# Kernel tuning notes

Measured on AMD Instinct MI355X. Metric: run time of the kernel, lower is better.

The kernel has to match this reference:

```python
import jax, jax.numpy as jnp
import numpy as np

B, T, C = 256, 2048, 39   # batch, time, nb_filters
NB = 8                     # number of dilation levels (2**0 .. 2**7)
K = 2                      # kernel size
NC = 8                     # num_classes
EPS = 1e-5                 # BatchNorm eps (eval mode)


def _causal_conv(x, w, b, d):
    """x: [B,C,T], w: [Cout,Cin,K], left-pad (K-1)*d for causality."""
    k = w.shape[-1]
    y = jax.lax.conv_general_dilated(
        x, w, window_strides=(1,), padding=[((k - 1) * d, 0)],
        rhs_dilation=(d,), dimension_numbers=('NCH', 'OIH', 'NCH'))
    return y + b[None, :, None]


def _bn(x, g, be, m, v):
    # eval-mode BatchNorm1d with running stats
    return g[None, :, None] * (x - m[None, :, None]) * jax.lax.rsqrt(v + EPS)[None, :, None] + be[None, :, None]


def _block(x, w, b, g, be, m, v, d):
    # Temporal_Aware_Block, eval mode (dropout = identity).
    # w: [2,C,C,K], b/g/be/m/v: [2,C]
    y = jax.nn.relu(_bn(_causal_conv(x, w[0], b[0], d), g[0], be[0], m[0], v[0]))
    y = jax.nn.relu(_bn(_causal_conv(y, w[1], b[1], d), g[1], be[1], m[1], v[1]))
    # causal conv preserves length, so the 1x1 residual conv branch is never taken
    return x * jax.nn.sigmoid(y)


def setup_inputs() -> dict:
    key = jax.random.key(0)
    ks = jax.random.split(key, 24)
    f = lambda k, s: jax.random.normal(k, s, dtype=jnp.float32) * 0.1
    return {
        'inputs': jax.random.normal(ks[0], (B, T, C), dtype=jnp.float32),
        'conv1x1_w': f(ks[1], (C, C, 1)),
        'conv1x1_b': f(ks[2], (C,)),
        'fw_conv_w': f(ks[3], (NB, 2, C, C, K)),
        'fw_conv_b': f(ks[4], (NB, 2, C)),
        'fw_gamma': 1.0 + f(ks[5], (NB, 2, C)),
        'fw_beta': f(ks[6], (NB, 2, C)),
        'fw_mean': f(ks[7], (NB, 2, C)),
        'fw_var': jax.random.uniform(ks[8], (NB, 2, C), dtype=jnp.float32, minval=0.5, maxval=1.5),
        'bw_conv_w': f(ks[9], (NB, 2, C, C, K)),
        'bw_conv_b': f(ks[10], (NB, 2, C)),
        'bw_gamma': 1.0 + f(ks[11], (NB, 2, C)),
        'bw_beta': f(ks[12], (NB, 2, C)),
        'bw_mean': f(ks[13], (NB, 2, C)),
        'bw_var': jax.random.uniform(ks[14], (NB, 2, C), dtype=jnp.float32, minval=0.5, maxval=1.5),
        'wl_kernel': f(ks[15], (NB, 1)),
        'cls_w': f(ks[16], (NC, C)),
        'cls_b': f(ks[17], (NC,)),
    }


def reference(inputs, conv1x1_w, conv1x1_b,
              fw_conv_w, fw_conv_b, fw_gamma, fw_beta, fw_mean, fw_var,
              bw_conv_w, bw_conv_b, bw_gamma, bw_beta, bw_mean, bw_var,
              wl_kernel, cls_w, cls_b):
    x = jnp.transpose(inputs, (0, 2, 1))           # [B,C,T]
    fwd = _causal_conv(x, conv1x1_w, conv1x1_b, 1)
    bwd = _causal_conv(x[:, :, ::-1], conv1x1_w, conv1x1_b, 1)
    skips = []
    for i in range(NB):
        d = 2 ** i
        fwd = _block(fwd, fw_conv_w[i], fw_conv_b[i], fw_gamma[i], fw_beta[i], fw_mean[i], fw_var[i], d)
        bwd = _block(bwd, bw_conv_w[i], bw_conv_b[i], bw_gamma[i], bw_beta[i], bw_mean[i], bw_var[i], d)
        skips.append(jnp.mean(fwd + bwd, axis=-1))  # [B,C]
    g = jnp.stack(skips, axis=-1)                   # [B,C,NB]
    x2 = jnp.einsum('bcn,no->bc', g, wl_kernel)     # WeightLayer matmul + squeeze
    logits = x2 @ cls_w.T + cls_b                   # [B,NC]
    return jax.nn.log_softmax(logits, axis=1)
```

## Files before the change

kernel.cpp:

```cpp
#include <hip/hip_runtime.h>
#include <math.h>

#define BATCH 256
#define TT    2048
#define CC    39
#define CP    40
#define NBLK  8
#define KK    2
#define NCLS  8
#define BN_EPS 1e-5f

typedef __attribute__((ext_vector_type(8))) short short8;
typedef __attribute__((ext_vector_type(4))) float floatx4;

__device__ __forceinline__ unsigned short f2b(float f) {
    union { float f; unsigned u; } v; v.f = f;
    unsigned r = v.u + 0x7FFF + ((v.u >> 16) & 1);
    return (unsigned short)(r >> 16);
}
__device__ __forceinline__ float b2f(unsigned short h) {
    union { unsigned u; float f; } v; v.u = ((unsigned)h) << 16;
    return v.f;
}

#define WFB_PER_BLKDIR (2*2*2*3*512)
#define WFB_TOTAL      (2*NBLK*WFB_PER_BLKDIR)
#define BFB_TOTAL      (2*NBLK*2*48)
#define WFF_TOTAL      (2*3*512)
#define BFF_TOTAL      48

__global__ void fold_kernel(const float* __restrict__ fw_w, const float* __restrict__ fw_b,
                            const float* __restrict__ fw_g, const float* __restrict__ fw_be,
                            const float* __restrict__ fw_m, const float* __restrict__ fw_v,
                            const float* __restrict__ bw_w, const float* __restrict__ bw_b,
                            const float* __restrict__ bw_g, const float* __restrict__ bw_be,
                            const float* __restrict__ bw_m, const float* __restrict__ bw_v,
                            const float* __restrict__ c1w, const float* __restrict__ c1b,
                            unsigned short* __restrict__ wfb, float* __restrict__ bfb,
                            unsigned short* __restrict__ wff, float* __restrict__ bff) {
    int idx = blockIdx.x * blockDim.x + threadIdx.x;
    if (idx < WFB_TOTAL) {
        int i = idx;
        int reg = i & 7;  i >>= 3;
        int lane = i & 63; i >>= 6;
        int n = i % 3;     i /= 3;
        int s = i & 1;     i >>= 1;
        int p = i & 1;     i >>= 1;
        int layer = i & 1; i >>= 1;
        int blk = i & 7;   i >>= 3;
        int dir = i;
        int co = n * 16 + (lane & 15);
        int ci = s * 32 + ((lane >> 4) << 3) + reg;
        float val = 0.f;
        if (co < CC && ci < CC) {
            const float* w = dir ? bw_w : fw_w;
            const float* g = dir ? bw_g : fw_g;
            const float* v = dir ? bw_v : fw_v;
            int il = blk * 2 + layer;
            float sc = g[il * CC + co] * rsqrtf(v[il * CC + co] + BN_EPS);
            val = w[((size_t)(il * CC + co) * CC + ci) * KK + p] * sc;
        }
        wfb[idx] = f2b(val);
        return;
    }
    idx -= WFB_TOTAL;
    if (idx < BFB_TOTAL) {
        int co = idx % 48;
        int i = idx / 48;
        int layer = i & 1; i >>= 1;
        int blk = i & 7;   i >>= 3;
        int dir = i;
        float val = 0.f;
        if (co < CC) {
            const float* b  = dir ? bw_b  : fw_b;
            const float* g  = dir ? bw_g  : fw_g;
            const float* be = dir ? bw_be : fw_be;
            const float* m  = dir ? bw_m  : fw_m;
            const float* v  = dir ? bw_v  : fw_v;
            int r = (blk * 2 + layer) * CC + co;
            float sc = g[r] * rsqrtf(v[r] + BN_EPS);
            val = (b[r] - m[r]) * sc + be[r];
        }
        bfb[idx] = val;
        return;
    }
    idx -= BFB_TOTAL;
    if (idx < WFF_TOTAL) {
        int i = idx;
        int reg = i & 7;  i >>= 3;
        int lane = i & 63; i >>= 6;
        int n = i % 3;     i /= 3;
        int s = i;
        int co = n * 16 + (lane & 15);
        int ci = s * 32 + ((lane >> 4) << 3) + reg;
        float val = (co < CC && ci < CC) ? c1w[co * CC + ci] : 0.f;
        wff[idx] = f2b(val);
        return;
    }
    idx -= WFF_TOTAL;
    if (idx < BFF_TOTAL) {
        bff[idx] = (idx < CC) ? c1b[idx] : 0.f;
    }
}

__global__ __launch_bounds__(256) void front_mfma(const float* __restrict__ in,
                                                  const unsigned short* __restrict__ wf,
                                                  const float* __restrict__ bias,
                                                  unsigned short* __restrict__ out) {
    __shared__ unsigned short xt[256 * CP + 32];
    const int dir = blockIdx.z, b = blockIdx.y, t0 = blockIdx.x * 256;
    const int tid = threadIdx.x, lane = tid & 63, wave = tid >> 6;
    const int stmin = dir ? (TT - t0 - 256) : t0;
    const float* src = in + ((size_t)b * TT + stmin) * CC;

    for (int e = tid; e < 256 * CC; e += 256) {
        int r = e / CC, c = e - r * CC;
        xt[r * CP + c] = f2b(src[e]);
    }
    if (tid < 256) xt[tid * CP + CC] = 0;
    if (tid < 32)  xt[256 * CP + tid] = 0;
    __syncthreads();

    short8 Wf[2][3];
#pragma unroll
    for (int s = 0; s < 2; ++s)
#pragma unroll
        for (int n = 0; n < 3; ++n)
            Wf[s][n] = *(const short8*)(wf + (((size_t)(s * 3 + n) * 64 + lane) << 3));
    float bias_n[3];
#pragma unroll
    for (int n = 0; n < 3; ++n) bias_n[n] = bias[n * 16 + (lane & 15)];

    for (int mt = wave; mt < 16; mt += 4) {
        int j0 = mt << 4;
        floatx4 acc[3];
#pragma unroll
        for (int n = 0; n < 3; ++n) acc[n] = floatx4{bias_n[n], bias_n[n], bias_n[n], bias_n[n]};
#pragma unroll
        for (int s = 0; s < 2; ++s) {
            short8 A = *(const short8*)(xt + (j0 + (lane & 15)) * CP + s * 32 + ((lane >> 4) << 3));
#pragma unroll
            for (int n = 0; n < 3; ++n)
                acc[n] = __builtin_amdgcn_mfma_f32_16x16x32_bf16(A, Wf[s][n], acc[n], 0, 0, 0);
        }
#pragma unroll
        for (int n = 0; n < 3; ++n) {
            int col = n * 16 + (lane & 15);
            if (col < CP) {
#pragma unroll
                for (int j = 0; j < 4; ++j) {
                    int r = j0 + ((lane >> 4) << 2) + j;
                    int t = dir ? (t0 + 255 - r) : (t0 + r);
                    out[((size_t)(dir * BATCH + b) * TT + t) * CP + col] = f2b(acc[n][j]);
                }
            }
        }
    }
}

__global__ __launch_bounds__(256) void block_mfma(const unsigned short* __restrict__ xg,
                                                  unsigned short* __restrict__ yg,
                                                  const unsigned short* __restrict__ wf_all,
                                                  const float* __restrict__ bf_all,
                                                  float* __restrict__ skipPart,
                                                  int d, int blk, int Tt, int writeOut) {
    extern __shared__ char ldsraw[];
    const int dir = blockIdx.z, b = blockIdx.y, tile = blockIdx.x;
    const int t0 = tile * Tt;
    const int tid = threadIdx.x, lane = tid & 63, wave = tid >> 6;
    const int rows_x = Tt + 2 * d;
    const int M1 = (Tt + d + 15) >> 4;
    const int rows_y1 = M1 << 4;
    const int rows_real = Tt + d;

    unsigned short* xt = (unsigned short*)ldsraw;
    unsigned short* y1 = xt + rows_x * CP + 32;
    float* stash = (float*)(y1 + rows_y1 * CP + 32);

    const size_t cbase = (size_t)(dir * BATCH + b) * TT * CP;
    const unsigned short* wf = wf_all + (size_t)(dir * NBLK + blk) * WFB_PER_BLKDIR;
    const float* bf = bf_all + (size_t)(dir * NBLK + blk) * 96;

    {
        const uint4* gsrc = (const uint4*)(xg + cbase);
        uint4* ldst = (uint4*)xt;
        int base_t = t0 - 2 * d;
        int nch = rows_x * 5;
        for (int c = tid; c < nch; c += 256) {
            int row = c / 5;
            int t = base_t + row;
            uint4 v;
            if (t < 0) { v.x = v.y = v.z = v.w = 0u; }
            else       { v = gsrc[(size_t)t * 5 + (c - row * 5)]; }
            ldst[c] = v;
        }
        if (tid < 16) ((unsigned*)(xt + rows_x * CP))[tid] = 0;
        if (tid >= 16 && tid < 32) ((unsigned*)(y1 + rows_y1 * CP))[tid - 16] = 0;
    }
    __syncthreads();

    short8 Wf[2][2][3];
#pragma unroll
    for (int p = 0; p < 2; ++p)
#pragma unroll
        for (int s = 0; s < 2; ++s)
#pragma unroll
            for (int n = 0; n < 3; ++n)
                Wf[p][s][n] = *(const short8*)(wf + (((size_t)(((0 * 2 + p) * 2 + s) * 3 + n) * 64 + lane) << 3));
    float bias0[3];
#pragma unroll
    for (int n = 0; n < 3; ++n) bias0[n] = bf[n * 16 + (lane & 15)];

    for (int mt = wave; mt < M1; mt += 4) {
        int j0 = mt << 4;
        floatx4 acc[3];
#pragma unroll
        for (int n = 0; n < 3; ++n) acc[n] = floatx4{bias0[n], bias0[n], bias0[n], bias0[n]};
#pragma unroll
        for (int p = 0; p < 2; ++p) {
            int rbase = j0 + (lane & 15) + (p ? d : 0);
#pragma unroll
            for (int s = 0; s < 2; ++s) {
                short8 A = *(const short8*)(xt + rbase * CP + s * 32 + ((lane >> 4) << 3));
#pragma unroll
                for (int n = 0; n < 3; ++n)
                    acc[n] = __builtin_amdgcn_mfma_f32_16x16x32_bf16(A, Wf[p][s][n], acc[n], 0, 0, 0);
            }
        }
#pragma unroll
        for (int n = 0; n < 3; ++n) {
            int col = n * 16 + (lane & 15);
            if (col < CP) {
#pragma unroll
                for (int j = 0; j < 4; ++j) {
                    int r = j0 + ((lane >> 4) << 2) + j;
                    int t = t0 - d + r;
                    float v = fmaxf(acc[n][j], 0.f);
                    if (t < 0 || r >= rows_real) v = 0.f;
                    y1[r * CP + col] = f2b(v);
                }
            }
        }
    }
    __syncthreads();

#pragma unroll
    for (int p = 0; p < 2; ++p)
#pragma unroll
        for (int s = 0; s < 2; ++s)
#pragma unroll
            for (int n = 0; n < 3; ++n)
                Wf[p][s][n] = *(const short8*)(wf + (((size_t)(((1 * 2 + p) * 2 + s) * 3 + n) * 64 + lane) << 3));
    float bias1[3];
#pragma unroll
    for (int n = 0; n < 3; ++n) bias1[n] = bf[48 + n * 16 + (lane & 15)];

    float sums[3] = {0.f, 0.f, 0.f};
    const int M2w = Tt >> 6;
    for (int mi = 0; mi < M2w; ++mi) {
        int j0 = (wave * M2w + mi) << 4;
        floatx4 acc[3];
#pragma unroll
        for (int n = 0; n < 3; ++n) acc[n] = floatx4{bias1[n], bias1[n], bias1[n], bias1[n]};
#pragma unroll
        for (int p = 0; p < 2; ++p) {
            int rbase = j0 + (lane & 15) + (p ? d : 0);
#pragma unroll
            for (int s = 0; s < 2; ++s) {
                short8 A = *(const short8*)(y1 + rbase * CP + s * 32 + ((lane >> 4) << 3));
#pragma unroll
                for (int n = 0; n < 3; ++n)
                    acc[n] = __builtin_amdgcn_mfma_f32_16x16x32_bf16(A, Wf[p][s][n], acc[n], 0, 0, 0);
            }
        }
#pragma unroll
        for (int n = 0; n < 3; ++n) {
            int col = n * 16 + (lane & 15);
#pragma unroll
            for (int j = 0; j < 4; ++j) {
                int r = j0 + ((lane >> 4) << 2) + j;
                float sig = 1.f / (1.f + __expf(-acc[n][j]));
                float xv = b2f(xt[(r + 2 * d) * CP + col]);
                float g = xv * sig;
                if (writeOut && col < CP)
                    yg[cbase + (size_t)(t0 + r) * CP + col] = f2b(g);
                sums[n] += g;
            }
        }
    }
#pragma unroll
    for (int n = 0; n < 3; ++n) {
        sums[n] += __shfl_xor(sums[n], 16, 64);
        sums[n] += __shfl_xor(sums[n], 32, 64);
    }
    if (lane < 16) {
#pragma unroll
        for (int n = 0; n < 3; ++n) stash[wave * 48 + n * 16 + lane] = sums[n];
    }
    __syncthreads();
    if (tid < CC) {
        float s = stash[tid] + stash[48 + tid] + stash[96 + tid] + stash[144 + tid];
        skipPart[(((size_t)(blk * 2 + dir) * BATCH + b) * CC + tid) * 16 + tile] = s;
    }
}

__global__ __launch_bounds__(64) void tail_kernel(const float* __restrict__ skipPart,
                                                  const float* __restrict__ wl,
                                                  const float* __restrict__ cw,
                                                  const float* __restrict__ cb,
                                                  float* __restrict__ out) {
    __shared__ float xs[CC];
    int b = blockIdx.x;
    int c = threadIdx.x;
    if (c < CC) {
        float x2 = 0.f;
        for (int i = 0; i < NBLK; ++i) {
            float wli = wl[i] * (1.0f / TT);
            int nt = (i == NBLK - 1) ? 16 : 8;
            for (int dirn = 0; dirn < 2; ++dirn) {
                const float* sp = skipPart + (((size_t)(i * 2 + dirn) * BATCH + b) * CC + c) * 16;
                float s = 0.f;
                for (int tl = 0; tl < nt; ++tl) s += sp[tl];
                x2 = fmaf(s, wli, x2);
            }
        }
        xs[c] = x2;
    }
    __syncthreads();
    if (threadIdx.x == 0) {
        float lg[NCLS];
        float mx = -1e30f;
        for (int o = 0; o < NCLS; ++o) {
            float a = cb[o];
#pragma unroll
            for (int cc2 = 0; cc2 < CC; ++cc2) a = fmaf(cw[o * CC + cc2], xs[cc2], a);
            lg[o] = a;
            mx = fmaxf(mx, a);
        }
        float se = 0.f;
        for (int o = 0; o < NCLS; ++o) se += expf(lg[o] - mx);
        float lse = logf(se) + mx;
        for (int o = 0; o < NCLS; ++o) out[b * NCLS + o] = lg[o] - lse;
    }
}

extern "C" void kernel_launch(void* const* d_in, const int* in_sizes, int n_in,
                              void* d_out, int out_size, void* d_ws, size_t ws_size,
                              hipStream_t stream) {
    const float* inputs = (const float*)d_in[0];
    const float* c1w    = (const float*)d_in[1];
    const float* c1b    = (const float*)d_in[2];
    const float* fw_w   = (const float*)d_in[3];
    const float* fw_b   = (const float*)d_in[4];
    const float* fw_g   = (const float*)d_in[5];
    const float* fw_be  = (const float*)d_in[6];
    const float* fw_m   = (const float*)d_in[7];
    const float* fw_v   = (const float*)d_in[8];
    const float* bw_w   = (const float*)d_in[9];
    const float* bw_b   = (const float*)d_in[10];
    const float* bw_g   = (const float*)d_in[11];
    const float* bw_be  = (const float*)d_in[12];
    const float* bw_m   = (const float*)d_in[13];
    const float* bw_v   = (const float*)d_in[14];
    const float* wl     = (const float*)d_in[15];
    const float* clsw   = (const float*)d_in[16];
    const float* clsb   = (const float*)d_in[17];

    const size_t bufsz = (size_t)2 * BATCH * TT * CP;
    unsigned short* buf0 = (unsigned short*)d_ws;
    unsigned short* buf1 = buf0 + bufsz;
    float* skip = (float*)(buf1 + bufsz);
    const size_t skipsz = (size_t)NBLK * 2 * BATCH * CC * 16;
    unsigned short* wfb = (unsigned short*)(skip + skipsz);
    float* bfb = (float*)(wfb + WFB_TOTAL);
    unsigned short* wff = (unsigned short*)(bfb + BFB_TOTAL);
    float* bff = (float*)(wff + WFF_TOTAL);

    {
        int tot = WFB_TOTAL + BFB_TOTAL + WFF_TOTAL + BFF_TOTAL;
        fold_kernel<<<(tot + 255) / 256, 256, 0, stream>>>(
            fw_w, fw_b, fw_g, fw_be, fw_m, fw_v,
            bw_w, bw_b, bw_g, bw_be, bw_m, bw_v, c1w, c1b,
            wfb, bfb, wff, bff);
    }

    front_mfma<<<dim3(TT / 256, BATCH, 2), 256, 0, stream>>>(inputs, wff, bff, buf0);

    unsigned short* cur = buf0;
    unsigned short* nxt = buf1;
    for (int i = 0; i < NBLK; ++i) {
        int d = 1 << i;
        int Tt = (d == 128) ? 128 : 256;
        int ntl = TT / Tt;
        int rows_x = Tt + 2 * d;
        int M1 = (Tt + d + 15) >> 4;
        int rows_y1 = M1 << 4;
        size_t lds = ((size_t)(rows_x * CP + 32) + (size_t)(rows_y1 * CP + 32)) * 2 + 4 * 48 * 4;
        block_mfma<<<dim3(ntl, BATCH, 2), 256, lds, stream>>>(
            cur, nxt, wfb, bfb, skip, d, i, Tt, (i < NBLK - 1) ? 1 : 0);
        unsigned short* tmp = cur; cur = nxt; nxt = tmp;
    }

    tail_kernel<<<BATCH, 64, 0, stream>>>(skip, wl, clsw, clsb, (float*)d_out);
}
```

Measured before the change: 657.9 us.

## Transpose MFMA operands and pack dilated taps into shared K dimension

The MFMA is restructured so weights become the A operand and activations the B operand. Each lane then holds four consecutive output channels for one time row, which allows packed bf16 stores via v_cvt_pk_bf16_f32 and vectorized residual loads instead of scalar per-element stores. The two causal taps are interleaved into the K dimension (lane groups select tap offset d), so each conv layer uses 3 K-slices instead of 2x2, cutting MFMAs per tile from 12 to 9. Sigmoid uses rcp, and the skip reduction and weight fold layout change to match.

```diff
diff --git a/kernel.cpp b/kernel.cpp
--- a/kernel.cpp
+++ b/kernel.cpp
@@ -18,16 +18,23 @@
     unsigned r = v.u + 0x7FFF + ((v.u >> 16) & 1);
     return (unsigned short)(r >> 16);
 }
-__device__ __forceinline__ float b2f(unsigned short h) {
-    union { unsigned u; float f; } v; v.u = ((unsigned)h) << 16;
-    return v.f;
-}
-
-#define WFB_PER_BLKDIR (2*2*2*3*512)
-#define WFB_TOTAL      (2*NBLK*WFB_PER_BLKDIR)
-#define BFB_TOTAL      (2*NBLK*2*48)
-#define WFF_TOTAL      (2*3*512)
-#define BFF_TOTAL      48
+__device__ __forceinline__ unsigned cvtpk(float lo, float hi) {
+    unsigned r;
+    asm("v_cvt_pk_bf16_f32 %0, %1, %2" : "=v"(r) : "v"(lo), "v"(hi));
+    return r;
+}
+__device__ __forceinline__ float blo(unsigned u) {
+    union { unsigned v; float f; } k; k.v = u << 16; return k.f;
+}
+__device__ __forceinline__ float bhi(unsigned u) {
+    union { unsigned v; float f; } k; k.v = u & 0xffff0000u; return k.f;
+}
+
+#define WFB_PER   (2*3*3*512)
+#define WFB_TOTAL (2*NBLK*WFB_PER)
+#define BFB_TOTAL (2*NBLK*2*48)
+#define WFF_TOTAL (3*2*512)
+#define BFF_TOTAL 48
 
 __global__ void fold_kernel(const float* __restrict__ fw_w, const float* __restrict__ fw_b,
                             const float* __restrict__ fw_g, const float* __restrict__ fw_be,
@@ -41,16 +48,17 @@
     int idx = blockIdx.x * blockDim.x + threadIdx.x;
     if (idx < WFB_TOTAL) {
         int i = idx;
-        int reg = i & 7;  i >>= 3;
+        int reg = i & 7;   i >>= 3;
         int lane = i & 63; i >>= 6;
-        int n = i % 3;     i /= 3;
-        int s = i & 1;     i >>= 1;
-        int p = i & 1;     i >>= 1;
+        int sl = i % 3;    i /= 3;
+        int ct = i % 3;    i /= 3;
         int layer = i & 1; i >>= 1;
         int blk = i & 7;   i >>= 3;
         int dir = i;
-        int co = n * 16 + (lane & 15);
-        int ci = s * 32 + ((lane >> 4) << 3) + reg;
+        int co = ct * 16 + (lane & 15);
+        int kin = ((lane >> 4) << 3) + reg;
+        int p = kin >> 4;
+        int ci = sl * 16 + (kin & 15);
         float val = 0.f;
         if (co < CC && ci < CC) {
             const float* w = dir ? bw_w : fw_w;
@@ -87,12 +95,12 @@
     idx -= BFB_TOTAL;
     if (idx < WFF_TOTAL) {
         int i = idx;
-        int reg = i & 7;  i >>= 3;
+        int reg = i & 7;   i >>= 3;
         int lane = i & 63; i >>= 6;
-        int n = i % 3;     i /= 3;
-        int s = i;
-        int co = n * 16 + (lane & 15);
-        int ci = s * 32 + ((lane >> 4) << 3) + reg;
+        int sl = i & 1;    i >>= 1;
+        int ct = i;
+        int co = ct * 16 + (lane & 15);
+        int ci = sl * 32 + ((lane >> 4) << 3) + reg;
         float val = (co < CC && ci < CC) ? c1w[co * CC + ci] : 0.f;
         wff[idx] = f2b(val);
         return;
@@ -110,50 +118,56 @@
     __shared__ unsigned short xt[256 * CP + 32];
     const int dir = blockIdx.z, b = blockIdx.y, t0 = blockIdx.x * 256;
     const int tid = threadIdx.x, lane = tid & 63, wave = tid >> 6;
+    const int c = lane & 15, g = lane >> 4;
     const int stmin = dir ? (TT - t0 - 256) : t0;
     const float* src = in + ((size_t)b * TT + stmin) * CC;
 
-    for (int e = tid; e < 256 * CC; e += 256) {
-        int r = e / CC, c = e - r * CC;
-        xt[r * CP + c] = f2b(src[e]);
-    }
-    if (tid < 256) xt[tid * CP + CC] = 0;
-    if (tid < 32)  xt[256 * CP + tid] = 0;
+    unsigned* xd = (unsigned*)xt;
+    for (int e = tid; e < 256 * 20; e += 256) {
+        int row = e / 20, cp = e - row * 20;
+        int c0 = cp * 2;
+        float f0 = src[(size_t)row * CC + c0];
+        float f1 = (c0 + 1 < CC) ? src[(size_t)row * CC + c0 + 1] : 0.f;
+        xd[row * 20 + cp] = cvtpk(f0, f1);
+    }
+    if (tid < 16) ((unsigned*)(xt + 256 * CP))[tid] = 0;
     __syncthreads();
 
-    short8 Wf[2][3];
-#pragma unroll
-    for (int s = 0; s < 2; ++s)
-#pragma unroll
-        for (int n = 0; n < 3; ++n)
-            Wf[s][n] = *(const short8*)(wf + (((size_t)(s * 3 + n) * 64 + lane) << 3));
-    float bias_n[3];
-#pragma unroll
-    for (int n = 0; n < 3; ++n) bias_n[n] = bias[n * 16 + (lane & 15)];
+    short8 Wf[3][2];
+#pragma unroll
+    for (int ct = 0; ct < 3; ++ct)
+#pragma unroll
+        for (int sl = 0; sl < 2; ++sl)
+            Wf[ct][sl] = *(const short8*)(wf + (((ct * 2 + sl) * 64 + lane) << 3));
+    float bs[3][4];
+#pragma unroll
+    for (int ct = 0; ct < 3; ++ct)
+#pragma unroll
+        for (int j = 0; j < 4; ++j) bs[ct][j] = bias[ct * 16 + g * 4 + j];
 
     for (int mt = wave; mt < 16; mt += 4) {
-        int j0 = mt << 4;
+        int row = (mt << 4) + c;
+        const unsigned short* bp = xt + row * CP;
         floatx4 acc[3];
 #pragma unroll
-        for (int n = 0; n < 3; ++n) acc[n] = floatx4{bias_n[n], bias_n[n], bias_n[n], bias_n[n]};
-#pragma unroll
-        for (int s = 0; s < 2; ++s) {
-            short8 A = *(const short8*)(xt + (j0 + (lane & 15)) * CP + s * 32 + ((lane >> 4) << 3));
-#pragma unroll
-            for (int n = 0; n < 3; ++n)
-                acc[n] = __builtin_amdgcn_mfma_f32_16x16x32_bf16(A, Wf[s][n], acc[n], 0, 0, 0);
-        }
-#pragma unroll
-        for (int n = 0; n < 3; ++n) {
-            int col = n * 16 + (lane & 15);
-            if (col < CP) {
-#pragma unroll
-                for (int j = 0; j < 4; ++j) {
-                    int r = j0 + ((lane >> 4) << 2) + j;
-                    int t = dir ? (t0 + 255 - r) : (t0 + r);
-                    out[((size_t)(dir * BATCH + b) * TT + t) * CP + col] = f2b(acc[n][j]);
-                }
-            }
+        for (int ct = 0; ct < 3; ++ct)
+            acc[ct] = floatx4{bs[ct][0], bs[ct][1], bs[ct][2], bs[ct][3]};
+#pragma unroll
+        for (int sl = 0; sl < 2; ++sl) {
+            short8 B = *(const short8*)(bp + sl * 32 + g * 8);
+#pragma unroll
+            for (int ct = 0; ct < 3; ++ct)
+                acc[ct] = __builtin_amdgcn_mfma_f32_16x16x32_bf16(Wf[ct][sl], B, acc[ct], 0, 0, 0);
+        }
+        int t = dir ? (t0 + 255 - row) : (t0 + row);
+        unsigned short* op = out + ((size_t)(dir * BATCH + b) * TT + t) * CP;
+#pragma unroll
+        for (int ct = 0; ct < 3; ++ct) {
+            if (ct == 2 && g >= 2) continue;
+            uint2 v;
+            v.x = cvtpk(acc[ct][0], acc[ct][1]);
+            v.y = cvtpk(acc[ct][2], acc[ct][3]);
+            *(uint2*)(op + ct * 16 + g * 4) = v;
         }
     }
 }
@@ -168,6 +182,9 @@
     const int dir = blockIdx.z, b = blockIdx.y, tile = blockIdx.x;
     const int t0 = tile * Tt;
     const int tid = threadIdx.x, lane = tid & 63, wave = tid >> 6;
+    const int c = lane & 15, g = lane >> 4;
+    const int tapoff = (g >> 1) ? d : 0;
+    const int koff8 = (g & 1) << 3;
     const int rows_x = Tt + 2 * d;
     const int M1 = (Tt + d + 15) >> 4;
     const int rows_y1 = M1 << 4;
@@ -178,7 +195,7 @@
     float* stash = (float*)(y1 + rows_y1 * CP + 32);
 
     const size_t cbase = (size_t)(dir * BATCH + b) * TT * CP;
-    const unsigned short* wf = wf_all + (size_t)(dir * NBLK + blk) * WFB_PER_BLKDIR;
+    const unsigned short* wf = wf_all + (size_t)(dir * NBLK + blk) * WFB_PER;
     const float* bf = bf_all + (size_t)(dir * NBLK + blk) * 96;
 
     {
@@ -186,116 +203,130 @@
         uint4* ldst = (uint4*)xt;
         int base_t = t0 - 2 * d;
         int nch = rows_x * 5;
-        for (int c = tid; c < nch; c += 256) {
-            int row = c / 5;
+        for (int ch = tid; ch < nch; ch += 256) {
+            int row = ch / 5;
             int t = base_t + row;
             uint4 v;
             if (t < 0) { v.x = v.y = v.z = v.w = 0u; }
-            else       { v = gsrc[(size_t)t * 5 + (c - row * 5)]; }
-            ldst[c] = v;
-        }
-        if (tid < 16) ((unsigned*)(xt + rows_x * CP))[tid] = 0;
-        if (tid >= 16 && tid < 32) ((unsigned*)(y1 + rows_y1 * CP))[tid - 16] = 0;
+            else       { v = gsrc[(size_t)t * 5 + (ch - row * 5)]; }
+            ldst[ch] = v;
+        }
+        if (tid < 16) ((unsigned*)(xt + (size_t)rows_x * CP))[tid] = 0;
+        else if (tid < 32) ((unsigned*)(y1 + (size_t)rows_y1 * CP))[tid - 16] = 0;
     }
     __syncthreads();
 
-    short8 Wf[2][2][3];
-#pragma unroll
-    for (int p = 0; p < 2; ++p)
-#pragma unroll
-        for (int s = 0; s < 2; ++s)
-#pragma unroll
-            for (int n = 0; n < 3; ++n)
-                Wf[p][s][n] = *(const short8*)(wf + (((size_t)(((0 * 2 + p) * 2 + s) * 3 + n) * 64 + lane) << 3));
-    float bias0[3];
-#pragma unroll
-    for (int n = 0; n < 3; ++n) bias0[n] = bf[n * 16 + (lane & 15)];
+    short8 Wf[3][3];
+#pragma unroll
+    for (int ct = 0; ct < 3; ++ct)
+#pragma unroll
+        for (int sl = 0; sl < 3; ++sl)
+            Wf[ct][sl] = *(const short8*)(wf + ((((0 * 3 + ct) * 3 + sl) * 64 + lane) << 3));
+    float bs[3][4];
+#pragma unroll
+    for (int ct = 0; ct < 3; ++ct)
+#pragma unroll
+        for (int j = 0; j < 4; ++j) bs[ct][j] = bf[ct * 16 + g * 4 + j];
 
     for (int mt = wave; mt < M1; mt += 4) {
         int j0 = mt << 4;
+        int brow = j0 + c + tapoff;
+        const unsigned short* bp = xt + brow * CP + koff8;
         floatx4 acc[3];
 #pragma unroll
-        for (int n = 0; n < 3; ++n) acc[n] = floatx4{bias0[n], bias0[n], bias0[n], bias0[n]};
-#pragma unroll
-        for (int p = 0; p < 2; ++p) {
-            int rbase = j0 + (lane & 15) + (p ? d : 0);
-#pragma unroll
-            for (int s = 0; s < 2; ++s) {
-                short8 A = *(const short8*)(xt + rbase * CP + s * 32 + ((lane >> 4) << 3));
-#pragma unroll
-                for (int n = 0; n < 3; ++n)
-                    acc[n] = __builtin_amdgcn_mfma_f32_16x16x32_bf16(A, Wf[p][s][n], acc[n], 0, 0, 0);
-            }
-        }
-#pragma unroll
-        for (int n = 0; n < 3; ++n) {
-            int col = n * 16 + (lane & 15);
-            if (col < CP) {
-#pragma unroll
-                for (int j = 0; j < 4; ++j) {
-                    int r = j0 + ((lane >> 4) << 2) + j;
-                    int t = t0 - d + r;
-                    float v = fmaxf(acc[n][j], 0.f);
-                    if (t < 0 || r >= rows_real) v = 0.f;
-                    y1[r * CP + col] = f2b(v);
-                }
-            }
+        for (int ct = 0; ct < 3; ++ct)
+            acc[ct] = floatx4{bs[ct][0], bs[ct][1], bs[ct][2], bs[ct][3]};
+#pragma unroll
+        for (int sl = 0; sl < 3; ++sl) {
+            short8 B = *(const short8*)(bp + sl * 16);
+#pragma unroll
+            for (int ct = 0; ct < 3; ++ct)
+                acc[ct] = __builtin_amdgcn_mfma_f32_16x16x32_bf16(Wf[ct][sl], B, acc[ct], 0, 0, 0);
+        }
+        int r = j0 + c;
+        bool dead = (t0 - d + r < 0) || (r >= rows_real);
+        unsigned short* yp = y1 + r * CP;
+#pragma unroll
+        for (int ct = 0; ct < 3; ++ct) {
+            if (ct == 2 && g >= 2) continue;
+            uint2 v;
+            v.x = cvtpk(fmaxf(acc[ct][0], 0.f), fmaxf(acc[ct][1], 0.f));
+            v.y = cvtpk(fmaxf(acc[ct][2], 0.f), fmaxf(acc[ct][3], 0.f));
+            if (dead) { v.x = 0u; v.y = 0u; }
+            *(uint2*)(yp + ct * 16 + g * 4) = v;
         }
     }
     __syncthreads();
 
 #pragma unroll
-    for (int p = 0; p < 2; ++p)
-#pragma unroll
-        for (int s = 0; s < 2; ++s)
-#pragma unroll
-            for (int n = 0; n < 3; ++n)
-                Wf[p][s][n] = *(const short8*)(wf + (((size_t)(((1 * 2 + p) * 2 + s) * 3 + n) * 64 + lane) << 3));
-    float bias1[3];
-#pragma unroll
-    for (int n = 0; n < 3; ++n) bias1[n] = bf[48 + n * 16 + (lane & 15)];
-
-    float sums[3] = {0.f, 0.f, 0.f};
+    for (int ct = 0; ct < 3; ++ct)
+#pragma unroll
+        for (int sl = 0; sl < 3; ++sl)
+            Wf[ct][sl] = *(const short8*)(wf + ((((1 * 3 + ct) * 3 + sl) * 64 + lane) << 3));
+#pragma unroll
+    for (int ct = 0; ct < 3; ++ct)
+#pragma unroll
+        for (int j = 0; j < 4; ++j) bs[ct][j] = bf[48 + ct * 16 + g * 4 + j];
+
+    float sums[3][4];
+#pragma unroll
+    for (int ct = 0; ct < 3; ++ct)
+#pragma unroll
+        for (int j = 0; j < 4; ++j) sums[ct][j] = 0.f;
+
     const int M2w = Tt >> 6;
     for (int mi = 0; mi < M2w; ++mi) {
         int j0 = (wave * M2w + mi) << 4;
+        int brow = j0 + c + tapoff;
+        const unsigned short* bp = y1 + brow * CP + koff8;
         floatx4 acc[3];
 #pragma unroll
-        for (int n = 0; n < 3; ++n) acc[n] = floatx4{bias1[n], bias1[n], bias1[n], bias1[n]};
-#pragma unroll
-        for (int p = 0; p < 2; ++p) {
-            int rbase = j0 + (lane & 15) + (p ? d : 0);
-#pragma unroll
-            for (int s = 0; s < 2; ++s) {
-                short8 A = *(const short8*)(y1 + rbase * CP + s * 32 + ((lane >> 4) << 3));
-#pragma unroll
-                for (int n = 0; n < 3; ++n)
-                    acc[n] = __builtin_amdgcn_mfma_f32_16x16x32_bf16(A, Wf[p][s][n], acc[n], 0, 0, 0);
+        for (int ct = 0; ct < 3; ++ct)
+            acc[ct] = floatx4{bs[ct][0], bs[ct][1], bs[ct][2], bs[ct][3]};
+#pragma unroll
+        for (int sl = 0; sl < 3; ++sl) {
+            short8 B = *(const short8*)(bp + sl * 16);
+#pragma unroll
+            for (int ct = 0; ct < 3; ++ct)
+                acc[ct] = __builtin_amdgcn_mfma_f32_16x16x32_bf16(Wf[ct][sl], B, acc[ct], 0, 0, 0);
+        }
+        int r = j0 + c;
+        const unsigned short* xrow = xt + (r + 2 * d) * CP;
+        unsigned short* orow = yg + cbase + (size_t)(t0 + r) * CP;
+#pragma unroll
+        for (int ct = 0; ct < 3; ++ct) {
+            uint2 xv = *(const uint2*)(xrow + ct * 16 + g * 4);
+            float g0 = blo(xv.x) * __builtin_amdgcn_rcpf(1.f + __expf(-acc[ct][0]));
+            float g1 = bhi(xv.x) * __builtin_amdgcn_rcpf(1.f + __expf(-acc[ct][1]));
+            float g2 = blo(xv.y) * __builtin_amdgcn_rcpf(1.f + __expf(-acc[ct][2]));
+            float g3 = bhi(xv.y) * __builtin_amdgcn_rcpf(1.f + __expf(-acc[ct][3]));
+            sums[ct][0] += g0; sums[ct][1] += g1;
+            sums[ct][2] += g2; sums[ct][3] += g3;
+            if (writeOut && !(ct == 2 && g >= 2)) {
+                uint2 v;
+                v.x = cvtpk(g0, g1);
+                v.y = cvtpk(g2, g3);
+                *(uint2*)(orow + ct * 16 + g * 4) = v;
             }
         }
-#pragma unroll
-        for (int n = 0; n < 3; ++n) {
-            int col = n * 16 + (lane & 15);
-#pragma unroll
-            for (int j = 0; j < 4; ++j) {
-                int r = j0 + ((lane >> 4) << 2) + j;
-                float sig = 1.f / (1.f + __expf(-acc[n][j]));
-                float xv = b2f(xt[(r + 2 * d) * CP + col]);
-                float g = xv * sig;
-                if (writeOut && col < CP)
-                    yg[cbase + (size_t)(t0 + r) * CP + col] = f2b(g);
-                sums[n] += g;
-            }
-        }
-    }
-#pragma unroll
-    for (int n = 0; n < 3; ++n) {
-        sums[n] += __shfl_xor(sums[n], 16, 64);
-        sums[n] += __shfl_xor(sums[n], 32, 64);
-    }
-    if (lane < 16) {
-#pragma unroll
-        for (int n = 0; n < 3; ++n) stash[wave * 48 + n * 16 + lane] = sums[n];
+    }
+#pragma unroll
+    for (int ct = 0; ct < 3; ++ct)
+#pragma unroll
+        for (int j = 0; j < 4; ++j) {
+            float v = sums[ct][j];
+            v += __shfl_xor(v, 1, 64);
+            v += __shfl_xor(v, 2, 64);
+            v += __shfl_xor(v, 4, 64);
+            v += __shfl_xor(v, 8, 64);
+            sums[ct][j] = v;
+        }
+    if (c == 0) {
+#pragma unroll
+        for (int ct = 0; ct < 3; ++ct)
+#pragma unroll
+            for (int j = 0; j < 4; ++j)
+                stash[wave * 48 + ct * 16 + g * 4 + j] = sums[ct][j];
     }
     __syncthreads();
     if (tid < CC) {
@@ -311,20 +342,20 @@
                                                   float* __restrict__ out) {
     __shared__ float xs[CC];
     int b = blockIdx.x;
-    int c = threadIdx.x;
-    if (c < CC) {
+    int cth = threadIdx.x;
+    if (cth < CC) {
         float x2 = 0.f;
         for (int i = 0; i < NBLK; ++i) {
             float wli = wl[i] * (1.0f / TT);
             int nt = (i == NBLK - 1) ? 16 : 8;
             for (int dirn = 0; dirn < 2; ++dirn) {
-                const float* sp = skipPart + (((size_t)(i * 2 + dirn) * BATCH + b) * CC + c) * 16;
+                const float* sp = skipPart + (((size_t)(i * 2 + dirn) * BATCH + b) * CC + cth) * 16;
                 float s = 0.f;
                 for (int tl = 0; tl < nt; ++tl) s += sp[tl];
                 x2 = fmaf(s, wli, x2);
             }
         }
-        xs[c] = x2;
+        xs[cth] = x2;
     }
     __syncthreads();
     if (threadIdx.x == 0) {
```

After: 543.3 us. -17.4%, faster.
